# Optimization experiments

Measured on AMD Instinct MI355X. Metric: run time of the kernel, lower is better.

Reference implementation:

```python
import jax, jax.numpy as jnp
import numpy as np

H, HKV, HD = 16, 4, 128
EPS = 1.1920928955078125e-07  # float32 eps, torch F.rms_norm default


def _rms_norm(t):
    return t * jax.lax.rsqrt(jnp.mean(t * t, axis=-1, keepdims=True) + EPS)


def _rope(t, cos, sin):
    # t: [B, T, h, HD]; cos/sin: [T, HD//2] -> broadcast [1, T, 1, HD//2]
    te, to = t[..., 0::2], t[..., 1::2]
    c = cos[None, :, None, :]
    s = sin[None, :, None, :]
    re = te * c - to * s
    ro = te * s + to * c
    return jnp.stack((re, ro), axis=-1).reshape(t.shape)


def setup_inputs() -> dict:
    key = jax.random.key(0)
    ks = jax.random.split(key, 5)
    B, T, C = 2, 2048, 2048
    return {
        "x": jax.random.normal(ks[0], (B, T, C), jnp.float32),
        "Wq": jax.random.normal(ks[1], (C, C), jnp.float32) * 0.02,
        "Wk": jax.random.normal(ks[2], (HKV * HD, C), jnp.float32) * 0.02,
        "Wv": jax.random.normal(ks[3], (HKV * HD, C), jnp.float32) * 0.02,
        "Wo": jax.random.normal(ks[4], (C, C), jnp.float32) * 0.02,
        "q_gain": jnp.full((H,), 5.0, jnp.float32),
    }


def reference(x, Wq, Wk, Wv, Wo, q_gain):
    B, T, C = x.shape
    q = (x @ Wq.T).reshape(B, T, H, HD)
    k = (x @ Wk.T).reshape(B, T, HKV, HD)
    v = (x @ Wv.T).reshape(B, T, HKV, HD)

    q = _rms_norm(q)
    k = _rms_norm(k)

    theta = 1.0 / (10000.0 ** (jnp.arange(0, HD, 2, dtype=jnp.float32) / HD))
    t = jnp.arange(T, dtype=jnp.float32)
    freqs = jnp.outer(t, theta)  # [T, HD//2]
    cos, sin = jnp.cos(freqs), jnp.sin(freqs)

    q = _rope(q, cos, sin)
    k = _rope(k, cos, sin)
    q = q * q_gain[None, None, :, None]

    qh = q.transpose(0, 2, 1, 3)                       # [B, H, T, HD]
    kh = jnp.repeat(k.transpose(0, 2, 1, 3), H // HKV, axis=1)
    vh = jnp.repeat(v.transpose(0, 2, 1, 3), H // HKV, axis=1)

    scale = 1.0 / jnp.sqrt(jnp.float32(HD))
    scores = jnp.einsum("bhqd,bhkd->bhqk", qh, kh) * scale
    causal = jnp.tril(jnp.ones((T, T), bool))
    scores = jnp.where(causal[None, None], scores, jnp.finfo(scores.dtype).min)
    attn = jax.nn.softmax(scores, axis=-1)
    out = jnp.einsum("bhqk,bhkd->bhqd", attn, vh)
    out = out.transpose(0, 2, 1, 3).reshape(B, T, C)
    return out @ Wo.T
```

## Files before the change

kernel.cpp:

```cpp
#include <hip/hip_runtime.h>
#include <hip/hip_bf16.h>

#define TSEQ 2048
#define CDIM 2048
#define NH   16
#define NKV  4
#define HDIM 128
#define BATCH 2
#define MROWS (BATCH*TSEQ)
#define KVC   (NKV*HDIM)
#define QKVC  (CDIM + 2*KVC)

typedef short bf16x8 __attribute__((ext_vector_type(8)));
typedef float f32x4  __attribute__((ext_vector_type(4)));

typedef const __attribute__((address_space(1))) void* gptr_t;
typedef __attribute__((address_space(3))) void* sptr_t;

__device__ inline void async16(const __hip_bfloat16* g, __hip_bfloat16* l) {
  __builtin_amdgcn_global_load_lds((gptr_t)g, (sptr_t)l, 16, 0, 0);
}

__device__ inline f32x4 mfma16(bf16x8 a, bf16x8 b, f32x4 c) {
  return __builtin_amdgcn_mfma_f32_16x16x32_bf16(a, b, c, 0, 0, 0);
}

__device__ inline float bfbits2f(unsigned short u) {
  return __uint_as_float(((unsigned)u) << 16);
}

__device__ inline unsigned short f2bfu(float x) {
  __hip_bfloat16 t = __float2bfloat16(x);
  return *(unsigned short*)&t;
}

__device__ inline bool detect_bf16(const void* x) {
  const unsigned short* u = (const unsigned short*)x;
  int lane = threadIdx.x & 63;
  int c = 0;
#pragma unroll
  for (int i = 0; i < 4; ++i) {
    float a = fabsf(bfbits2f(u[(lane*4 + i)*2]));
    if (a >= 1e-6f && a <= 1e3f) c++;
  }
#pragma unroll
  for (int off = 32; off >= 1; off >>= 1) c += __shfl_xor(c, off);
  return c > 128;
}

__device__ inline int swz128(int row, int col) {
  return row*128 + (((col >> 3) ^ (row & 15)) << 3) + (col & 7);
}
__device__ inline int swz64(int row, int col) {
  return row*64 + ((((col >> 3) ^ row) & 7) << 3) + (col & 7);
}

__global__ __launch_bounds__(256) void canonize_all(
    const void* __restrict__ xs,  const void* __restrict__ wqs,
    const void* __restrict__ wks, const void* __restrict__ wvs,
    const void* __restrict__ wos, const void* __restrict__ gs,
    __hip_bfloat16* __restrict__ xd,
    __hip_bfloat16* __restrict__ wqkv,
    __hip_bfloat16* __restrict__ wod,
    __hip_bfloat16* __restrict__ gd)
{
  const bool isbf = detect_bf16(xs);
  int blk = blockIdx.x;
  const void* src; __hip_bfloat16* dst; int base, n;
  if      (blk < 4096) { src = xs;  dst = xd;                base = blk;        n = MROWS*CDIM; }
  else if (blk < 6144) { src = wqs; dst = wqkv;              base = blk - 4096; n = CDIM*CDIM; }
  else if (blk < 6656) { src = wks; dst = wqkv + (size_t)CDIM*CDIM;            base = blk - 6144; n = KVC*CDIM; }
  else if (blk < 7168) { src = wvs; dst = wqkv + (size_t)(CDIM+KVC)*CDIM;      base = blk - 6656; n = KVC*CDIM; }
  else if (blk < 9216) { src = wos; dst = wod;               base = blk - 7168; n = CDIM*CDIM; }
  else                 { src = gs;  dst = gd;                base = 0;          n = NH; }
  int idx = base*2048 + threadIdx.x*8;
  if (idx >= n) return;
  if (isbf) {
    *(bf16x8*)&dst[idx] = *(const bf16x8*)((const __hip_bfloat16*)src + idx);
  } else {
    const float* s = (const float*)src + idx;
    float4 f0 = *(const float4*)s;
    float4 f1 = *(const float4*)(s + 4);
    union { bf16x8 v; unsigned short u[8]; } o;
    o.u[0] = f2bfu(f0.x); o.u[1] = f2bfu(f0.y);
    o.u[2] = f2bfu(f0.z); o.u[3] = f2bfu(f0.w);
    o.u[4] = f2bfu(f1.x); o.u[5] = f2bfu(f1.y);
    o.u[6] = f2bfu(f1.z); o.u[7] = f2bfu(f1.w);
    *(bf16x8*)&dst[idx] = o.v;
  }
}

#define BK 64

__global__ __launch_bounds__(512, 2) void gemm_bt256(
    const __hip_bfloat16* __restrict__ A,
    const __hip_bfloat16* __restrict__ B,
    __hip_bfloat16* __restrict__ C,
    int M, int N, int K, int lda)
{
  __shared__ __align__(16) __hip_bfloat16 As[3][256*BK];
  __shared__ __align__(16) __hip_bfloat16 Bs[2][192*BK];
  const int tid  = threadIdx.x;
  const int wave = tid >> 6;
  const int lane = tid & 63;
  const int qd   = lane >> 4;
  const int ln   = lane & 15;
  const int m0   = blockIdx.y * 256;
  const int n0   = blockIdx.x * 192;
  const int wm   = (wave >> 2) * 128;
  const int wn   = (wave & 3) * 48;

  auto stageAhalf = [&](int buf, int kt, int half) {
    const __hip_bfloat16* src = A + (size_t)(m0 + half*128)*lda + kt*BK;
    __hip_bfloat16* dst = &As[buf][half*128*BK];
#pragma unroll
    for (int i = 0; i < 2; ++i) {
      int c = i*512 + tid;
      int row = c >> 3, sl = c & 7;
      int gs = sl ^ (row & 7);
      async16(&src[(size_t)row*lda + gs*8], &dst[(i*512 + wave*64)*8]);
    }
  };
  auto stageB = [&](int buf, int kt) {
    const __hip_bfloat16* src = B + (size_t)n0*K + kt*BK;
    __hip_bfloat16* dst = &Bs[buf][0];
#pragma unroll
    for (int i = 0; i < 3; ++i) {
      int c = i*512 + tid;
      int row = c >> 3, sl = c & 7;
      int gs = sl ^ (row & 7);
      async16(&src[(size_t)row*K + gs*8], &dst[(i*512 + wave*64)*8]);
    }
  };
  auto ldA = [&](int buf, int m, int kk) -> bf16x8 {
    int row = wm + m*16 + ln;
    return *(const bf16x8*)&As[buf][row*BK + (((kk*4 + qd) ^ (row & 7)) << 3)];
  };
  auto ldB = [&](int buf, int n, int kk) -> bf16x8 {
    int row = wn + n*16 + ln;
    return *(const bf16x8*)&Bs[buf][row*BK + (((kk*4 + qd) ^ (row & 7)) << 3)];
  };

  f32x4 acc[8][3] = {};
  const int nt = K / BK;

  stageAhalf(0, 0, 0); stageAhalf(0, 0, 1); stageB(0, 0);
  if (nt > 1) {
    stageAhalf(1, 1, 0); stageAhalf(1, 1, 1); stageB(1, 1);
    asm volatile("s_waitcnt vmcnt(7)" ::: "memory");
  } else {
    asm volatile("s_waitcnt vmcnt(0)" ::: "memory");
  }
  __builtin_amdgcn_s_barrier();

#pragma unroll 1
  for (int t = 0; t < nt; ++t) {
    const int bufA = t % 3;
    const int bufB = t & 1;
    int nextA = bufA + 2; if (nextA >= 3) nextA -= 3;
    const bool pre = (t + 2 < nt);
    bf16x8 a03[4][2], a47[4][2], b01[2][2], b2[2];

#pragma unroll
    for (int m = 0; m < 4; ++m)
#pragma unroll
      for (int kk = 0; kk < 2; ++kk) a03[m][kk] = ldA(bufA, m, kk);
#pragma unroll
    for (int n = 0; n < 2; ++n)
#pragma unroll
      for (int kk = 0; kk < 2; ++kk) b01[n][kk] = ldB(bufB, n, kk);
    if (pre) stageAhalf(nextA, t + 2, 0);
    __builtin_amdgcn_s_setprio(1);
#pragma unroll
    for (int m = 0; m < 4; ++m)
#pragma unroll
      for (int n = 0; n < 2; ++n)
#pragma unroll
        for (int kk = 0; kk < 2; ++kk)
          acc[m][n] = mfma16(a03[m][kk], b01[n][kk], acc[m][n]);
    __builtin_amdgcn_s_setprio(0);
    __builtin_amdgcn_s_barrier();

#pragma unroll
    for (int m = 0; m < 4; ++m)
#pragma unroll
      for (int kk = 0; kk < 2; ++kk) a47[m][kk] = ldA(bufA, 4 + m, kk);
    if (pre) stageAhalf(nextA, t + 2, 1);
    __builtin_amdgcn_s_setprio(1);
#pragma unroll
    for (int m = 0; m < 4; ++m)
#pragma unroll
      for (int n = 0; n < 2; ++n)
#pragma unroll
        for (int kk = 0; kk < 2; ++kk)
          acc[4 + m][n] = mfma16(a47[m][kk], b01[n][kk], acc[4 + m][n]);
    __builtin_amdgcn_s_setprio(0);
    __builtin_amdgcn_s_barrier();

#pragma unroll
    for (int kk = 0; kk < 2; ++kk) b2[kk] = ldB(bufB, 2, kk);
    __builtin_amdgcn_s_setprio(1);
#pragma unroll
    for (int m = 0; m < 4; ++m)
#pragma unroll
      for (int kk = 0; kk < 2; ++kk)
        acc[m][2] = mfma16(a03[m][kk], b2[kk], acc[m][2]);
    __builtin_amdgcn_s_setprio(0);
    __builtin_amdgcn_s_barrier();

    if (pre) stageB(bufB, t + 2);
    __builtin_amdgcn_s_setprio(1);
#pragma unroll
    for (int m = 0; m < 4; ++m)
#pragma unroll
      for (int kk = 0; kk < 2; ++kk)
        acc[4 + m][2] = mfma16(a47[m][kk], b2[kk], acc[4 + m][2]);
    __builtin_amdgcn_s_setprio(0);
    if (pre) asm volatile("s_waitcnt vmcnt(7)" ::: "memory");
    else     asm volatile("s_waitcnt vmcnt(0)" ::: "memory");
    __builtin_amdgcn_s_barrier();
  }

#pragma unroll
  for (int m = 0; m < 8; ++m)
#pragma unroll
    for (int n = 0; n < 3; ++n) {
      int row = m0 + wm + m*16 + qd*4;
      int col = n0 + wn + n*16 + ln;
#pragma unroll
      for (int r = 0; r < 4; ++r)
        C[(size_t)(row + r)*N + col] = __float2bfloat16(acc[m][n][r]);
    }
}

__global__ __launch_bounds__(256, 2) void gemm_out(
    const __hip_bfloat16* __restrict__ A,
    const __hip_bfloat16* __restrict__ B,
    void* __restrict__ C,
    int M, int N, int K, int lda, const void* __restrict__ xorig)
{
  const bool isbf = detect_bf16(xorig);
  __shared__ __align__(16) __hip_bfloat16 As[128*32];
  __shared__ __align__(16) __hip_bfloat16 Bs[128*32];
  const int tid  = threadIdx.x;
  const int wave = tid >> 6;
  const int lane = tid & 63;
  const int qd   = lane >> 4;
  const int ln   = lane & 15;
  const int m0   = blockIdx.y * 128;
  const int n0   = blockIdx.x * 128;
  const int wm   = (wave >> 1) * 64;
  const int wn   = (wave & 1) * 64;

  f32x4 acc[4][4] = {};

  for (int k0 = 0; k0 < K; k0 += 32) {
    __syncthreads();
#pragma unroll
    for (int r = 0; r < 2; ++r) {
      int e   = (r*256 + tid) * 8;
      int row = e >> 5;
      int col = e & 31;
      async16(&A[(size_t)(m0+row)*lda + k0 + col], &As[(size_t)(r*256 + wave*64)*8]);
      async16(&B[(size_t)(n0+row)*K   + k0 + col], &Bs[(size_t)(r*256 + wave*64)*8]);
    }
    __syncthreads();
    bf16x8 af[4], bfr[4];
#pragma unroll
    for (int i = 0; i < 4; ++i)
      af[i] = *(const bf16x8*)&As[(wm + i*16 + ln)*32 + qd*8];
#pragma unroll
    for (int j = 0; j < 4; ++j)
      bfr[j] = *(const bf16x8*)&Bs[(wn + j*16 + ln)*32 + qd*8];
#pragma unroll
    for (int i = 0; i < 4; ++i)
#pragma unroll
      for (int j = 0; j < 4; ++j)
        acc[i][j] = mfma16(af[i], bfr[j], acc[i][j]);
  }
#pragma unroll
  for (int i = 0; i < 4; ++i)
#pragma unroll
    for (int j = 0; j < 4; ++j) {
      int row = m0 + wm + i*16 + qd*4;
      int col = n0 + wn + j*16 + ln;
#pragma unroll
      for (int r = 0; r < 4; ++r) {
        if (isbf) ((__hip_bfloat16*)C)[(size_t)(row + r)*N + col] = __float2bfloat16(acc[i][j][r]);
        else      ((float*)C)[(size_t)(row + r)*N + col] = acc[i][j][r];
      }
    }
}

__global__ __launch_bounds__(256) void prep_and_tv(
    __hip_bfloat16* __restrict__ qkv,
    const __hip_bfloat16* __restrict__ gain,
    __hip_bfloat16* __restrict__ vt)
{
  int blk = blockIdx.x;
  if (blk < 10240) {
    int wid2 = blk * 4 + (threadIdx.x >> 6);
    int lane = threadIdx.x & 63;
    int half = lane >> 5;
    int l32  = lane & 31;
    int rowid = wid2 * 2 + half;
    bool isq = rowid < MROWS*NH;
    int m, h;
    __hip_bfloat16* p;
    if (isq) { m = rowid >> 4; h = rowid & 15; p = qkv + (size_t)m*QKVC + h*HDIM; }
    else     { int w2 = rowid - MROWS*NH; m = w2 >> 2; h = w2 & 3; p = qkv + (size_t)m*QKVC + CDIM + h*HDIM; }

    ushort4 raw = *(const ushort4*)((const unsigned short*)p + 4*l32);
    float e0 = bfbits2f(raw.x), o0 = bfbits2f(raw.y);
    float e1 = bfbits2f(raw.z), o1 = bfbits2f(raw.w);
    float ss = (e0*e0 + o0*o0) + (e1*e1 + o1*o1);
#pragma unroll
    for (int off = 16; off >= 1; off >>= 1) ss += __shfl_xor(ss, off);
    float rms = rsqrtf(ss * (1.0f/128.0f) + 1.1920928955078125e-07f);
    e0 *= rms; o0 *= rms; e1 *= rms; o1 *= rms;

    int j0 = 2*l32;
    float th0 = exp2f(-(float)(2*j0)     * (1.0f/128.0f) * 13.287712379549449f);
    float th1 = exp2f(-(float)(2*j0 + 2) * (1.0f/128.0f) * 13.287712379549449f);
    int t = m & (TSEQ-1);
    float fr0 = (float)t * th0, fr1 = (float)t * th1;
    float c0 = cosf(fr0), s0 = sinf(fr0);
    float c1 = cosf(fr1), s1 = sinf(fr1);
    float re0 = e0*c0 - o0*s0, ro0 = e0*s0 + o0*c0;
    float re1 = e1*c1 - o1*s1, ro1 = e1*s1 + o1*c1;

    if (isq) {
      float g = bfbits2f(*(const unsigned short*)&gain[h]) * 0.08838834764831845f;
      re0 *= g; ro0 *= g; re1 *= g; ro1 *= g;
    }
    ushort4 outv;
    outv.x = f2bfu(re0); outv.y = f2bfu(ro0);
    outv.z = f2bfu(re1); outv.w = f2bfu(ro1);
    *(ushort4*)((unsigned short*)p + 4*l32) = outv;
  } else {
    __shared__ __hip_bfloat16 tile[32][34];
    int bx = blk - 10240;
    int tx = threadIdx.x & 31;
    int ty = threadIdx.x >> 5;
    int r0 = (bx & 127) * 32;
    int c0 = (bx >> 7) * 32;
#pragma unroll
    for (int i = 0; i < 4; ++i)
      tile[ty + i*8][tx] = qkv[(size_t)(r0 + ty + i*8)*QKVC + (CDIM + KVC) + c0 + tx];
    __syncthreads();
    int b = r0 >> 11;
    int t = r0 & (TSEQ-1);
    int hk = c0 >> 7;
    int d0 = c0 & (HDIM-1);
#pragma unroll
    for (int i = 0; i < 4; ++i) {
      int d = d0 + ty + i*8;
      vt[((size_t)((b*NKV + hk)*HDIM + d))*TSEQ + t + tx] = tile[tx][ty + i*8];
    }
  }
}

__global__ __launch_bounds__(256, 2) void attn_kernel(
    const __hip_bfloat16* __restrict__ qkv,
    const __hip_bfloat16* __restrict__ vt,
    __hip_bfloat16* __restrict__ out)
{
  const int tid  = threadIdx.x;
  const int wave = tid >> 6;
  const int lane = tid & 63;
  const int qd = lane >> 4, ln = lane & 15;
  const int p  = blockIdx.x;
  const int h  = blockIdx.y;
  const int b  = blockIdx.z;
  const int hk = h >> 2;

  const __hip_bfloat16* K = qkv + (size_t)(b*TSEQ)*QKVC + CDIM + hk*HDIM;
  const __hip_bfloat16* V = vt + ((size_t)(b*NKV + hk)*HDIM)*TSEQ;

  __shared__ __align__(16) __hip_bfloat16 Ks[64*128];
  __shared__ __align__(16) __hip_bfloat16 Vs[128*64];
  __shared__ __align__(16) __hip_bfloat16 Pb[64*64];
  __shared__ float Lb[4][64];

  auto issueK = [&](int t0) {
#pragma unroll
    for (int i = 0; i < 4; ++i) {
      int c = i*256 + tid;
      int row = c >> 4, cc = c & 15;
      int gcc = cc ^ (row & 15);
      async16(&K[(size_t)(t0 + row)*QKVC + gcc*8], &Ks[(i*256 + wave*64)*8]);
    }
  };
  auto issueV = [&](int t0) {
#pragma unroll
    for (int i = 0; i < 4; ++i) {
      int c = i*256 + tid;
      int row = c >> 3, cc = c & 7;
      int gcc = cc ^ (row & 7);
      async16(&V[(size_t)row*TSEQ + t0 + gcc*8], &Vs[(i*256 + wave*64)*8]);
    }
  };

#pragma unroll 1
  for (int seg = 0; seg < 2; ++seg) {
    const int qt = seg ? (31 - p) : p;
    const int q0 = qt * 64;

    bf16x8 qfr[4][4];
#pragma unroll
    for (int qsub = 0; qsub < 4; ++qsub)
#pragma unroll
      for (int kc = 0; kc < 4; ++kc)
        qfr[qsub][kc] = *(const bf16x8*)&qkv[((size_t)(b*TSEQ + q0 + qsub*16 + ln))*QKVC + h*HDIM + kc*32 + qd*8];

    f32x4 o[2][4] = {};
    float lacc[4] = {0.f, 0.f, 0.f, 0.f};

    __syncthreads();
    issueK(0);
    __syncthreads();

#pragma unroll 1
    for (int kt = 0; kt <= qt; ++kt) {
      const int t0 = kt * 64;
      issueV(t0);

      f32x4 sc[4] = {};
#pragma unroll
      for (int kc = 0; kc < 4; ++kc) {
        bf16x8 kfa = *(const bf16x8*)&Ks[swz128(wave*16 + ln, kc*32 + qd*8)];
#pragma unroll
        for (int qsub = 0; qsub < 4; ++qsub)
          sc[qsub] = mfma16(kfa, qfr[qsub][kc], sc[qsub]);
      }
      if (kt == qt) {
#pragma unroll
        for (int qsub = 0; qsub < 4; ++qsub)
#pragma unroll
          for (int r = 0; r < 4; ++r) {
            int kv = t0 + wave*16 + qd*4 + r;
            int q  = q0 + qsub*16 + ln;
            if (kv > q) sc[qsub][r] = -1.0e30f;
          }
      }
#pragma unroll
      for (int qsub = 0; qsub < 4; ++qsub) {
#pragma unroll
        for (int r = 0; r < 4; ++r)
          sc[qsub][r] = __expf(sc[qsub][r]);
        lacc[qsub] += (sc[qsub][0] + sc[qsub][1]) + (sc[qsub][2] + sc[qsub][3]);
      }

#pragma unroll
      for (int qsub = 0; qsub < 4; ++qsub) {
        ushort4 pk;
        pk.x = f2bfu(sc[qsub][0]); pk.y = f2bfu(sc[qsub][1]);
        pk.z = f2bfu(sc[qsub][2]); pk.w = f2bfu(sc[qsub][3]);
        *(ushort4*)&Pb[swz64(qsub*16 + ln, wave*16 + qd*4)] = pk;
      }

      __syncthreads();
      if (kt < qt) issueK(t0 + 64);

      __builtin_amdgcn_s_setprio(1);
#pragma unroll
      for (int kc2 = 0; kc2 < 2; ++kc2) {
        bf16x8 pfb[4];
#pragma unroll
        for (int qsub = 0; qsub < 4; ++qsub)
          pfb[qsub] = *(const bf16x8*)&Pb[swz64(qsub*16 + ln, kc2*32 + qd*8)];
#pragma unroll
        for (int half = 0; half < 2; ++half) {
          bf16x8 vfa = *(const bf16x8*)&Vs[swz64(wave*32 + half*16 + ln, kc2*32 + qd*8)];
#pragma unroll
          for (int qsub = 0; qsub < 4; ++qsub)
            o[half][qsub] = mfma16(vfa, pfb[qsub], o[half][qsub]);
        }
      }
      __builtin_amdgcn_s_setprio(0);
      __syncthreads();
    }

#pragma unroll
    for (int qsub = 0; qsub < 4; ++qsub) {
      lacc[qsub] += __shfl_xor(lacc[qsub], 16);
      lacc[qsub] += __shfl_xor(lacc[qsub], 32);
    }
    if (qd == 0) {
#pragma unroll
      for (int qsub = 0; qsub < 4; ++qsub)
        Lb[wave][qsub*16 + ln] = lacc[qsub];
    }
    __syncthreads();
    float inv[4];
#pragma unroll
    for (int qsub = 0; qsub < 4; ++qsub) {
      int q = qsub*16 + ln;
      inv[qsub] = 1.0f / (((Lb[0][q] + Lb[1][q]) + (Lb[2][q] + Lb[3][q])));
    }

#pragma unroll
    for (int half = 0; half < 2; ++half)
#pragma unroll
      for (int qsub = 0; qsub < 4; ++qsub) {
        ushort4 pk;
        pk.x = f2bfu(o[half][qsub][0] * inv[qsub]);
        pk.y = f2bfu(o[half][qsub][1] * inv[qsub]);
        pk.z = f2bfu(o[half][qsub][2] * inv[qsub]);
        pk.w = f2bfu(o[half][qsub][3] * inv[qsub]);
        *(ushort4*)&Ks[swz128(qsub*16 + ln, wave*32 + half*16 + qd*4)] = pk;
      }
    __syncthreads();
#pragma unroll
    for (int pass = 0; pass < 4; ++pass) {
      int row = wave*16 + pass*4 + qd;
      bf16x8 val = *(const bf16x8*)&Ks[swz128(row, ln*8)];
      int q = q0 + row;
      *(bf16x8*)&out[((size_t)(b*TSEQ + q))*CDIM + h*HDIM + ln*8] = val;
    }
  }
}

extern "C" void kernel_launch(void* const* d_in, const int* in_sizes, int n_in,
                              void* d_out, int out_size, void* d_ws, size_t ws_size,
                              hipStream_t stream) {
  char* ws = (char*)d_ws;
  size_t off = 0;
  auto alloc = [&](size_t bytes) { char* p = ws + off; off += (bytes + 255) & ~(size_t)255; return p; };

  __hip_bfloat16* xb   = (__hip_bfloat16*)alloc((size_t)MROWS*CDIM*2);
  __hip_bfloat16* wqkv = (__hip_bfloat16*)alloc((size_t)QKVC*CDIM*2);
  __hip_bfloat16* wob  = (__hip_bfloat16*)alloc((size_t)CDIM*CDIM*2);
  __hip_bfloat16* gb   = (__hip_bfloat16*)alloc(256);
  __hip_bfloat16* qkv  = (__hip_bfloat16*)alloc((size_t)MROWS*QKVC*2);
  __hip_bfloat16* vt   = (__hip_bfloat16*)alloc((size_t)MROWS*KVC*2);

  canonize_all<<<9217, 256, 0, stream>>>(
      d_in[0], d_in[1], d_in[2], d_in[3], d_in[4], d_in[5],
      xb, wqkv, wob, gb);

  gemm_bt256<<<dim3(QKVC/192, MROWS/256), 512, 0, stream>>>(
      xb, wqkv, qkv, MROWS, QKVC, CDIM, CDIM);

  prep_and_tv<<<12288, 256, 0, stream>>>(qkv, gb, vt);

  attn_kernel<<<dim3(16, NH, BATCH), 256, 0, stream>>>(qkv, vt, xb);

  gemm_out<<<dim3(CDIM/128, MROWS/128), 256, 0, stream>>>(
      xb, wob, d_out, MROWS, CDIM, CDIM, CDIM, d_in[0]);
}
```

Before: 284.6 us.

## Fuse V transpose into QKV GEMM epilogue and pipeline output projection GEMM

```diff
diff --git a/kernel.cpp b/kernel.cpp
--- a/kernel.cpp
+++ b/kernel.cpp
@@ -96,6 +96,7 @@
     const __hip_bfloat16* __restrict__ A,
     const __hip_bfloat16* __restrict__ B,
     __hip_bfloat16* __restrict__ C,
+    __hip_bfloat16* __restrict__ vt,
     int M, int N, int K, int lda)
 {
   __shared__ __align__(16) __hip_bfloat16 As[3][256*BK];
@@ -227,137 +228,202 @@
     for (int n = 0; n < 3; ++n) {
       int row = m0 + wm + m*16 + qd*4;
       int col = n0 + wn + n*16 + ln;
-#pragma unroll
-      for (int r = 0; r < 4; ++r)
-        C[(size_t)(row + r)*N + col] = __float2bfloat16(acc[m][n][r]);
-    }
-}
-
-__global__ __launch_bounds__(256, 2) void gemm_out(
+      if (col < CDIM + KVC) {
+#pragma unroll
+        for (int r = 0; r < 4; ++r)
+          C[(size_t)(row + r)*N + col] = __float2bfloat16(acc[m][n][r]);
+      } else {
+        int cv = col - (CDIM + KVC);
+        int hk = cv >> 7, d = cv & (HDIM-1);
+        int bb = row >> 11, tt = row & (TSEQ-1);
+        ushort4 pk;
+        pk.x = f2bfu(acc[m][n][0]); pk.y = f2bfu(acc[m][n][1]);
+        pk.z = f2bfu(acc[m][n][2]); pk.w = f2bfu(acc[m][n][3]);
+        *(ushort4*)&vt[(((size_t)(bb*NKV + hk))*HDIM + d)*TSEQ + tt] = pk;
+      }
+    }
+}
+
+__global__ __launch_bounds__(512, 2) void gemm_out(
     const __hip_bfloat16* __restrict__ A,
     const __hip_bfloat16* __restrict__ B,
     void* __restrict__ C,
     int M, int N, int K, int lda, const void* __restrict__ xorig)
 {
   const bool isbf = detect_bf16(xorig);
-  __shared__ __align__(16) __hip_bfloat16 As[128*32];
-  __shared__ __align__(16) __hip_bfloat16 Bs[128*32];
+  __shared__ __align__(16) __hip_bfloat16 As[3][256*BK];
+  __shared__ __align__(16) __hip_bfloat16 Bs[2][128*BK];
   const int tid  = threadIdx.x;
   const int wave = tid >> 6;
   const int lane = tid & 63;
   const int qd   = lane >> 4;
   const int ln   = lane & 15;
-  const int m0   = blockIdx.y * 128;
+  const int m0   = blockIdx.y * 256;
   const int n0   = blockIdx.x * 128;
-  const int wm   = (wave >> 1) * 64;
-  const int wn   = (wave & 1) * 64;
-
-  f32x4 acc[4][4] = {};
-
-  for (int k0 = 0; k0 < K; k0 += 32) {
-    __syncthreads();
-#pragma unroll
-    for (int r = 0; r < 2; ++r) {
-      int e   = (r*256 + tid) * 8;
-      int row = e >> 5;
-      int col = e & 31;
-      async16(&A[(size_t)(m0+row)*lda + k0 + col], &As[(size_t)(r*256 + wave*64)*8]);
-      async16(&B[(size_t)(n0+row)*K   + k0 + col], &Bs[(size_t)(r*256 + wave*64)*8]);
-    }
-    __syncthreads();
-    bf16x8 af[4], bfr[4];
-#pragma unroll
-    for (int i = 0; i < 4; ++i)
-      af[i] = *(const bf16x8*)&As[(wm + i*16 + ln)*32 + qd*8];
-#pragma unroll
-    for (int j = 0; j < 4; ++j)
-      bfr[j] = *(const bf16x8*)&Bs[(wn + j*16 + ln)*32 + qd*8];
-#pragma unroll
-    for (int i = 0; i < 4; ++i)
-#pragma unroll
-      for (int j = 0; j < 4; ++j)
-        acc[i][j] = mfma16(af[i], bfr[j], acc[i][j]);
-  }
-#pragma unroll
-  for (int i = 0; i < 4; ++i)
-#pragma unroll
-    for (int j = 0; j < 4; ++j) {
-      int row = m0 + wm + i*16 + qd*4;
-      int col = n0 + wn + j*16 + ln;
+  const int wm   = (wave >> 2) * 128;
+  const int wn   = (wave & 3) * 32;
+
+  auto stageAhalf = [&](int buf, int kt, int half) {
+    const __hip_bfloat16* src = A + (size_t)(m0 + half*128)*lda + kt*BK;
+    __hip_bfloat16* dst = &As[buf][half*128*BK];
+#pragma unroll
+    for (int i = 0; i < 2; ++i) {
+      int c = i*512 + tid;
+      int row = c >> 3, sl = c & 7;
+      int gs = sl ^ (row & 7);
+      async16(&src[(size_t)row*lda + gs*8], &dst[(i*512 + wave*64)*8]);
+    }
+  };
+  auto stageB = [&](int buf, int kt) {
+    const __hip_bfloat16* src = B + (size_t)n0*K + kt*BK;
+    __hip_bfloat16* dst = &Bs[buf][0];
+#pragma unroll
+    for (int i = 0; i < 2; ++i) {
+      int c = i*512 + tid;
+      int row = c >> 3, sl = c & 7;
+      int gs = sl ^ (row & 7);
+      async16(&src[(size_t)row*K + gs*8], &dst[(i*512 + wave*64)*8]);
+    }
+  };
+  auto ldA = [&](int buf, int m, int kk) -> bf16x8 {
+    int row = wm + m*16 + ln;
+    return *(const bf16x8*)&As[buf][row*BK + (((kk*4 + qd) ^ (row & 7)) << 3)];
+  };
+  auto ldB = [&](int buf, int n, int kk) -> bf16x8 {
+    int row = wn + n*16 + ln;
+    return *(const bf16x8*)&Bs[buf][row*BK + (((kk*4 + qd) ^ (row & 7)) << 3)];
+  };
+
+  f32x4 acc[8][2] = {};
+  const int nt = K / BK;
+
+  stageAhalf(0, 0, 0); stageAhalf(0, 0, 1); stageB(0, 0);
+  if (nt > 1) {
+    stageAhalf(1, 1, 0); stageAhalf(1, 1, 1); stageB(1, 1);
+    asm volatile("s_waitcnt vmcnt(6)" ::: "memory");
+  } else {
+    asm volatile("s_waitcnt vmcnt(0)" ::: "memory");
+  }
+  __builtin_amdgcn_s_barrier();
+
+#pragma unroll 1
+  for (int t = 0; t < nt; ++t) {
+    const int bufA = t % 3;
+    const int bufB = t & 1;
+    int nextA = bufA + 2; if (nextA >= 3) nextA -= 3;
+    const bool pre = (t + 2 < nt);
+    bf16x8 a03[4][2], a47[4][2], bn0[2], bn1[2];
+
+#pragma unroll
+    for (int m = 0; m < 4; ++m)
+#pragma unroll
+      for (int kk = 0; kk < 2; ++kk) a03[m][kk] = ldA(bufA, m, kk);
+#pragma unroll
+    for (int kk = 0; kk < 2; ++kk) bn0[kk] = ldB(bufB, 0, kk);
+    if (pre) stageAhalf(nextA, t + 2, 0);
+    __builtin_amdgcn_s_setprio(1);
+#pragma unroll
+    for (int m = 0; m < 4; ++m)
+#pragma unroll
+      for (int kk = 0; kk < 2; ++kk)
+        acc[m][0] = mfma16(a03[m][kk], bn0[kk], acc[m][0]);
+    __builtin_amdgcn_s_setprio(0);
+    __builtin_amdgcn_s_barrier();
+
+#pragma unroll
+    for (int m = 0; m < 4; ++m)
+#pragma unroll
+      for (int kk = 0; kk < 2; ++kk) a47[m][kk] = ldA(bufA, 4 + m, kk);
+#pragma unroll
+    for (int kk = 0; kk < 2; ++kk) bn1[kk] = ldB(bufB, 1, kk);
+    if (pre) stageAhalf(nextA, t + 2, 1);
+    __builtin_amdgcn_s_setprio(1);
+#pragma unroll
+    for (int m = 0; m < 4; ++m)
+#pragma unroll
+      for (int kk = 0; kk < 2; ++kk)
+        acc[4 + m][0] = mfma16(a47[m][kk], bn0[kk], acc[4 + m][0]);
+    __builtin_amdgcn_s_setprio(0);
+    __builtin_amdgcn_s_barrier();
+
+    __builtin_amdgcn_s_setprio(1);
+#pragma unroll
+    for (int m = 0; m < 4; ++m)
+#pragma unroll
+      for (int kk = 0; kk < 2; ++kk)
+        acc[m][1] = mfma16(a03[m][kk], bn1[kk], acc[m][1]);
+    __builtin_amdgcn_s_setprio(0);
+    __builtin_amdgcn_s_barrier();
+
+    if (pre) stageB(bufB, t + 2);
+    __builtin_amdgcn_s_setprio(1);
+#pragma unroll
+    for (int m = 0; m < 4; ++m)
+#pragma unroll
+      for (int kk = 0; kk < 2; ++kk)
+        acc[4 + m][1] = mfma16(a47[m][kk], bn1[kk], acc[4 + m][1]);
+    __builtin_amdgcn_s_setprio(0);
+    if (pre) asm volatile("s_waitcnt vmcnt(6)" ::: "memory");
+    else     asm volatile("s_waitcnt vmcnt(0)" ::: "memory");
+    __builtin_amdgcn_s_barrier();
+  }
+
+#pragma unroll
+  for (int m = 0; m < 8; ++m)
+#pragma unroll
+    for (int n = 0; n < 2; ++n) {
+      int row = m0 + wm + m*16 + qd*4;
+      int col = n0 + wn + n*16 + ln;
 #pragma unroll
       for (int r = 0; r < 4; ++r) {
-        if (isbf) ((__hip_bfloat16*)C)[(size_t)(row + r)*N + col] = __float2bfloat16(acc[i][j][r]);
-        else      ((float*)C)[(size_t)(row + r)*N + col] = acc[i][j][r];
-      }
-    }
-}
-
-__global__ __launch_bounds__(256) void prep_and_tv(
+        if (isbf) ((__hip_bfloat16*)C)[(size_t)(row + r)*N + col] = __float2bfloat16(acc[m][n][r]);
+        else      ((float*)C)[(size_t)(row + r)*N + col] = acc[m][n][r];
+      }
+    }
+}
+
+__global__ __launch_bounds__(256) void prep_qk(
     __hip_bfloat16* __restrict__ qkv,
-    const __hip_bfloat16* __restrict__ gain,
-    __hip_bfloat16* __restrict__ vt)
+    const __hip_bfloat16* __restrict__ gain)
 {
-  int blk = blockIdx.x;
-  if (blk < 10240) {
-    int wid2 = blk * 4 + (threadIdx.x >> 6);
-    int lane = threadIdx.x & 63;
-    int half = lane >> 5;
-    int l32  = lane & 31;
-    int rowid = wid2 * 2 + half;
-    bool isq = rowid < MROWS*NH;
-    int m, h;
-    __hip_bfloat16* p;
-    if (isq) { m = rowid >> 4; h = rowid & 15; p = qkv + (size_t)m*QKVC + h*HDIM; }
-    else     { int w2 = rowid - MROWS*NH; m = w2 >> 2; h = w2 & 3; p = qkv + (size_t)m*QKVC + CDIM + h*HDIM; }
-
-    ushort4 raw = *(const ushort4*)((const unsigned short*)p + 4*l32);
-    float e0 = bfbits2f(raw.x), o0 = bfbits2f(raw.y);
-    float e1 = bfbits2f(raw.z), o1 = bfbits2f(raw.w);
-    float ss = (e0*e0 + o0*o0) + (e1*e1 + o1*o1);
-#pragma unroll
-    for (int off = 16; off >= 1; off >>= 1) ss += __shfl_xor(ss, off);
-    float rms = rsqrtf(ss * (1.0f/128.0f) + 1.1920928955078125e-07f);
-    e0 *= rms; o0 *= rms; e1 *= rms; o1 *= rms;
-
-    int j0 = 2*l32;
-    float th0 = exp2f(-(float)(2*j0)     * (1.0f/128.0f) * 13.287712379549449f);
-    float th1 = exp2f(-(float)(2*j0 + 2) * (1.0f/128.0f) * 13.287712379549449f);
-    int t = m & (TSEQ-1);
-    float fr0 = (float)t * th0, fr1 = (float)t * th1;
-    float c0 = cosf(fr0), s0 = sinf(fr0);
-    float c1 = cosf(fr1), s1 = sinf(fr1);
-    float re0 = e0*c0 - o0*s0, ro0 = e0*s0 + o0*c0;
-    float re1 = e1*c1 - o1*s1, ro1 = e1*s1 + o1*c1;
-
-    if (isq) {
-      float g = bfbits2f(*(const unsigned short*)&gain[h]) * 0.08838834764831845f;
-      re0 *= g; ro0 *= g; re1 *= g; ro1 *= g;
-    }
-    ushort4 outv;
-    outv.x = f2bfu(re0); outv.y = f2bfu(ro0);
-    outv.z = f2bfu(re1); outv.w = f2bfu(ro1);
-    *(ushort4*)((unsigned short*)p + 4*l32) = outv;
-  } else {
-    __shared__ __hip_bfloat16 tile[32][34];
-    int bx = blk - 10240;
-    int tx = threadIdx.x & 31;
-    int ty = threadIdx.x >> 5;
-    int r0 = (bx & 127) * 32;
-    int c0 = (bx >> 7) * 32;
-#pragma unroll
-    for (int i = 0; i < 4; ++i)
-      tile[ty + i*8][tx] = qkv[(size_t)(r0 + ty + i*8)*QKVC + (CDIM + KVC) + c0 + tx];
-    __syncthreads();
-    int b = r0 >> 11;
-    int t = r0 & (TSEQ-1);
-    int hk = c0 >> 7;
-    int d0 = c0 & (HDIM-1);
-#pragma unroll
-    for (int i = 0; i < 4; ++i) {
-      int d = d0 + ty + i*8;
-      vt[((size_t)((b*NKV + hk)*HDIM + d))*TSEQ + t + tx] = tile[tx][ty + i*8];
-    }
-  }
+  int wid2 = blockIdx.x * 4 + (threadIdx.x >> 6);
+  int lane = threadIdx.x & 63;
+  int half = lane >> 5;
+  int l32  = lane & 31;
+  int rowid = wid2 * 2 + half;
+  bool isq = rowid < MROWS*NH;
+  int m, h;
+  __hip_bfloat16* p;
+  if (isq) { m = rowid >> 4; h = rowid & 15; p = qkv + (size_t)m*QKVC + h*HDIM; }
+  else     { int w2 = rowid - MROWS*NH; m = w2 >> 2; h = w2 & 3; p = qkv + (size_t)m*QKVC + CDIM + h*HDIM; }
+
+  ushort4 raw = *(const ushort4*)((const unsigned short*)p + 4*l32);
+  float e0 = bfbits2f(raw.x), o0 = bfbits2f(raw.y);
+  float e1 = bfbits2f(raw.z), o1 = bfbits2f(raw.w);
+  float ss = (e0*e0 + o0*o0) + (e1*e1 + o1*o1);
+#pragma unroll
+  for (int off = 16; off >= 1; off >>= 1) ss += __shfl_xor(ss, off);
+  float rms = rsqrtf(ss * (1.0f/128.0f) + 1.1920928955078125e-07f);
+  e0 *= rms; o0 *= rms; e1 *= rms; o1 *= rms;
+
+  int j0 = 2*l32;
+  float th0 = exp2f(-(float)(2*j0)     * (1.0f/128.0f) * 13.287712379549449f);
+  float th1 = exp2f(-(float)(2*j0 + 2) * (1.0f/128.0f) * 13.287712379549449f);
+  int t = m & (TSEQ-1);
+  float fr0 = (float)t * th0, fr1 = (float)t * th1;
+  float c0 = cosf(fr0), s0 = sinf(fr0);
+  float c1 = cosf(fr1), s1 = sinf(fr1);
+  float re0 = e0*c0 - o0*s0, ro0 = e0*s0 + o0*c0;
+  float re1 = e1*c1 - o1*s1, ro1 = e1*s1 + o1*c1;
+
+  if (isq) {
+    float g = bfbits2f(*(const unsigned short*)&gain[h]) * 0.08838834764831845f;
+    re0 *= g; ro0 *= g; re1 *= g; ro1 *= g;
+  }
+  ushort4 outv;
+  outv.x = f2bfu(re0); outv.y = f2bfu(ro0);
+  outv.z = f2bfu(re1); outv.w = f2bfu(ro1);
+  *(ushort4*)((unsigned short*)p + 4*l32) = outv;
 }
 
 __global__ __launch_bounds__(256, 2) void attn_kernel(
@@ -540,12 +606,12 @@
       xb, wqkv, wob, gb);
 
   gemm_bt256<<<dim3(QKVC/192, MROWS/256), 512, 0, stream>>>(
-      xb, wqkv, qkv, MROWS, QKVC, CDIM, CDIM);
-
-  prep_and_tv<<<12288, 256, 0, stream>>>(qkv, gb, vt);
+      xb, wqkv, qkv, vt, MROWS, QKVC, CDIM, CDIM);
+
+  prep_qk<<<10240, 256, 0, stream>>>(qkv, gb);
 
   attn_kernel<<<dim3(16, NH, BATCH), 256, 0, stream>>>(qkv, vt, xb);
 
-  gemm_out<<<dim3(CDIM/128, MROWS/128), 256, 0, stream>>>(
+  gemm_out<<<dim3(CDIM/128, MROWS/256), 512, 0, stream>>>(
       xb, wob, d_out, MROWS, CDIM, CDIM, CDIM, d_in[0]);
 }
```

New measurement: 288.8 us. No clear change (+1.4%).
